# Kernel optimization log

Hardware: AMD Instinct MI355X
Metric: run time of the kernel (lower is better)

The kernel has to match this reference:

```python
import jax, jax.numpy as jnp
import numpy as np


def setup_inputs() -> dict:
    key = jax.random.key(0)
    ks = jax.random.split(key, 8)
    B, C, H, W = 4, 256, 56, 56
    Cq = C // 8
    s = 0.05  # small init scale for conv weights, like kaiming-ish for 1x1 convs
    return {
        "x": jax.random.normal(ks[0], (B, C, H, W), jnp.float32),
        "Wq": jax.random.normal(ks[1], (Cq, C), jnp.float32) * s,
        "bq": jax.random.normal(ks[2], (Cq,), jnp.float32) * s,
        "Wk": jax.random.normal(ks[3], (Cq, C), jnp.float32) * s,
        "bk": jax.random.normal(ks[4], (Cq,), jnp.float32) * s,
        "Wv": jax.random.normal(ks[5], (C, C), jnp.float32) * s,
        "bv": jax.random.normal(ks[6], (C,), jnp.float32) * s,
        "gamma": jax.random.normal(ks[7], (1,), jnp.float32),
    }


def reference(x, Wq, bq, Wk, bk, Wv, bv, gamma):
    B, C, H, W = x.shape
    N = H * W
    xf = x.reshape(B, C, N)  # flatten spatial

    # 1x1 convs == channel matmuls
    q = jnp.einsum('oc,bcn->bon', Wq, xf) + bq[None, :, None]   # [B,Cq,N]
    k = jnp.einsum('oc,bcn->bon', Wk, xf) + bk[None, :, None]   # [B,Cq,N]
    v = jnp.einsum('oc,bcn->bon', Wv, xf) + bv[None, :, None]   # [B,C,N]

    # lipschitz_norm from weights: u=||Q||_F, v=max row-norm of K^T, w=max row-norm of V^T
    u = jnp.linalg.norm(Wq)
    vn = jnp.max(jnp.linalg.norm(Wk.T, axis=1))
    wn = jnp.max(jnp.linalg.norm(Wv.T, axis=1))
    norm_value = jnp.maximum(u * vn, u * wn)  # maximum(u*v, v*u, u*w)

    # energy[b,i,j] = <q[:,i], k[:,j]>, scaled by custom Lipschitz norm
    energy = jnp.einsum('bci,bcj->bij', q, k) / norm_value      # [B,N,N]
    attention = jax.nn.softmax(energy, axis=-1)

    # out[b,c,i] = sum_j v[b,c,j] * attention[b,i,j]
    out = jnp.einsum('bcj,bij->bci', v, attention).reshape(B, C, H, W)

    # lipschitz_bound: exp(sqrt(3)) * sqrt(N/C) + 2*sqrt(6)
    bound = np.float32(np.exp(np.sqrt(3.0)) * np.sqrt(N / C) + 2.0 * np.sqrt(6.0))
    out = out / bound

    return gamma * out + x
```

## Files before the change

kernel.cpp:

```cpp
#include <hip/hip_runtime.h>

#define N_SP 3136
#define C_CH 256
#define CQ   32
#define NB   4
#define JT   64
#define NJT  49
#define QT   64
#define INV_BOUND 0.04051569f
#define LOG2E 1.44269504f

typedef __attribute__((ext_vector_type(8))) short bf16x8;
typedef __attribute__((ext_vector_type(4))) float f32x4;
typedef __attribute__((ext_vector_type(2))) long long l64x2;
typedef unsigned short u16;
typedef unsigned int   u32;
typedef unsigned char  u8;
typedef long long      l64;

#define MFMA16(a,b,c) __builtin_amdgcn_mfma_f32_16x16x32_bf16(a,b,c,0,0,0)
#define MFMA8(a,b,c)  __builtin_amdgcn_mfma_f32_16x16x32_bf8_fp8(a,b,c,0,0,0)

__device__ __forceinline__ u16 f2b(float f) {
    u32 u = __builtin_bit_cast(u32, f);
    u += 0x7fffu + ((u >> 16) & 1u);
    return (u16)(u >> 16);
}
__device__ __forceinline__ u8 f2fp8(float f) {
    return (u8)(__builtin_amdgcn_cvt_pk_fp8_f32(f, f, 0, false) & 0xff);
}
__device__ __forceinline__ void dma16(const void* g, void* l) {
    __builtin_amdgcn_global_load_lds((const __attribute__((address_space(1))) u32*)g,
                                     (__attribute__((address_space(3))) u32*)l, 16, 0, 0);
}

__global__ __launch_bounds__(256) void stage1_kernel(
    const float* __restrict__ x, const float* __restrict__ Wq,
    const float* __restrict__ Wk, const float* __restrict__ Wv,
    u8* __restrict__ xT, u8* __restrict__ Wqb, u8* __restrict__ Wkb,
    u8* __restrict__ Wvb, float* __restrict__ scale_out,
    float* __restrict__ kmax)
{
    __shared__ float smem[64 * 65];
    const int t = threadIdx.x;
    const int bid = blockIdx.x;

    if (bid < 784) {
        float (*tile)[65] = (float(*)[65])smem;
        const int xcd = bid & 7, slot = bid >> 3;
        const int b = xcd >> 1;
        const int i = slot * 2 + (xcd & 1);
        const int ct = i & 3, nt = i >> 2;
        const int c0 = ct * 64, n0 = nt * 64;
        const int cc = t >> 4, nn4 = (t & 15) * 4;
        #pragma unroll
        for (int k = 0; k < 4; ++k) {
            int cl = cc + k * 16;
            float4 v = *(const float4*)(x + (size_t)(b * C_CH + c0 + cl) * N_SP + n0 + nn4);
            tile[cl][nn4] = v.x; tile[cl][nn4 + 1] = v.y;
            tile[cl][nn4 + 2] = v.z; tile[cl][nn4 + 3] = v.w;
        }
        __syncthreads();
        const int c4 = (t & 15) * 4, nn = t >> 4;
        #pragma unroll
        for (int k = 0; k < 4; ++k) {
            int nl = nn + k * 16;
            ushort4 o;
            o.x = f2b(tile[c4 + 0][nl]); o.y = f2b(tile[c4 + 1][nl]);
            o.z = f2b(tile[c4 + 2][nl]); o.w = f2b(tile[c4 + 3][nl]);
            const int off = ((c0 + c4) * 2) ^ ((nl & 15) << 5);
            *(ushort4*)(xT + (size_t)(b * N_SP + n0 + nl) * 512 + off) = o;
        }
    } else if (bid < 864) {
        int idx = (bid - 784) * 256 + t;
        const float* src; u8* dst; int off;
        if (idx < 2048)      { src = Wq; dst = Wqb; off = idx; }
        else if (idx < 4096) { src = Wk; dst = Wkb; off = idx - 2048; }
        else                 { src = Wv; dst = Wvb; off = idx - 4096; }
        float4 v = *(const float4*)(src + off * 4);
        ushort4 o; o.x = f2b(v.x); o.y = f2b(v.y); o.z = f2b(v.z); o.w = f2b(v.w);
        const int row = off >> 6, inner = (off & 63) * 8;
        *(ushort4*)(dst + row * 512 + (inner ^ ((row & 15) << 5))) = o;
    } else {
        if (t < NB) kmax[t] = 0.f;
        float* red = smem;
        float u2 = 0.f;
        for (int i = t; i < CQ * C_CH; i += 256) { float w = Wq[i]; u2 += w * w; }
        red[t] = u2; __syncthreads();
        #pragma unroll
        for (int s = 128; s > 0; s >>= 1) { if (t < s) red[t] += red[t + s]; __syncthreads(); }
        float u2t = red[0]; __syncthreads();
        float vn2 = 0.f;
        for (int o = 0; o < CQ; ++o)   { float w = Wk[o * C_CH + t]; vn2 += w * w; }
        float wn2 = 0.f;
        for (int o = 0; o < C_CH; ++o) { float w = Wv[o * C_CH + t]; wn2 += w * w; }
        red[t] = fmaxf(vn2, wn2); __syncthreads();
        #pragma unroll
        for (int s = 128; s > 0; s >>= 1) { if (t < s) red[t] = fmaxf(red[t], red[t + s]); __syncthreads(); }
        if (t == 0) scale_out[0] = 1.0f / (sqrtf(u2t) * sqrtf(red[0]));
    }
}

__global__ __launch_bounds__(256) void qkv_mfma(
    const u8* __restrict__ xT, const u8* __restrict__ Wqb,
    const u8* __restrict__ Wkb, const u8* __restrict__ Wvb,
    const float* __restrict__ bq, const float* __restrict__ bk,
    const float* __restrict__ bv, const float* __restrict__ scale_p,
    u16* __restrict__ qT, u8* __restrict__ Kg, u8* __restrict__ Vg,
    float* __restrict__ qnorm, float* __restrict__ kmax)
{
    __shared__ __align__(16) u8 xTl[32768];
    __shared__ __align__(16) u8 Wl[32768];

    const int t = threadIdx.x;
    const int xcd = blockIdx.x & 7, slot = blockIdx.x >> 3;
    const int b = xcd >> 1;
    const int i = slot * 2 + (xcd & 1);
    if (i >= 245) return;
    const int split = i / 49, nt = i % 49;
    const int w = t >> 6, lane = t & 63, li = t & 15, g = (t >> 4) & 3;
    const int n = nt * 64 + w * 16 + li;
    const int r0 = (split - 1) * 64;
    const f32x4 zero = {0.f, 0.f, 0.f, 0.f};

    {
        const u8* xsrc = xT + (size_t)(b * N_SP + nt * 64) * 512;
        #pragma unroll
        for (int k = 0; k < 8; ++k)
            dma16(xsrc + w * 8192 + k * 1024 + lane * 16, xTl + w * 8192 + k * 1024);
        if (split == 0) {
            #pragma unroll
            for (int k = 0; k < 4; ++k)
                dma16(Wqb + w * 4096 + k * 1024 + lane * 16, Wl + w * 4096 + k * 1024);
            #pragma unroll
            for (int k = 0; k < 4; ++k)
                dma16(Wkb + w * 4096 + k * 1024 + lane * 16, Wl + 16384 + w * 4096 + k * 1024);
        } else {
            const u8* wsrc = Wvb + (size_t)r0 * 512;
            #pragma unroll
            for (int k = 0; k < 8; ++k)
                dma16(wsrc + w * 8192 + k * 1024 + lane * 16, Wl + w * 8192 + k * 1024);
        }
    }
    asm volatile("s_waitcnt vmcnt(0)" ::: "memory");
    __syncthreads();

    const int swz = li << 5;
    bf16x8 xf[8];
    #pragma unroll
    for (int ks = 0; ks < 8; ++ks)
        xf[ks] = *(const bf16x8*)(xTl + (w * 16 + li) * 512 + ((ks * 64 + 16 * g) ^ swz));

    if (split == 0) {
        f32x4 aq0 = zero, aq1 = zero, ak0 = zero, ak1 = zero;
        #pragma unroll
        for (int ks = 0; ks < 8; ++ks) {
            const int o = (ks * 64 + 16 * g) ^ swz;
            bf16x8 w0 = *(const bf16x8*)(Wl + li * 512 + o);
            bf16x8 w1 = *(const bf16x8*)(Wl + (16 + li) * 512 + o);
            bf16x8 w2 = *(const bf16x8*)(Wl + 16384 + li * 512 + o);
            bf16x8 w3 = *(const bf16x8*)(Wl + 16384 + (16 + li) * 512 + o);
            aq0 = MFMA16(w0, xf[ks], aq0);
            aq1 = MFMA16(w1, xf[ks], aq1);
            ak0 = MFMA16(w2, xf[ks], ak0);
            ak1 = MFMA16(w3, xf[ks], ak1);
        }
        const float scf = scale_p[0] * LOG2E;
        f32x4 bq0 = *(const f32x4*)(bq + 4 * g);
        f32x4 bq1 = *(const f32x4*)(bq + 16 + 4 * g);
        f32x4 bk0 = *(const f32x4*)(bk + 4 * g);
        f32x4 bk1 = *(const f32x4*)(bk + 16 + 4 * g);
        float qn2 = 0.f, kn2 = 0.f;
        ushort4 s0, s1;
        #pragma unroll
        for (int r = 0; r < 4; ++r) {
            float q0 = (aq0[r] + bq0[r]) * scf;
            float q1 = (aq1[r] + bq1[r]) * scf;
            qn2 += q0 * q0 + q1 * q1;
            ((u16*)&s0)[r] = f2b(q0); ((u16*)&s1)[r] = f2b(q1);
        }
        *(ushort4*)(qT + (size_t)(b * N_SP + n) * CQ + 4 * g)      = s0;
        *(ushort4*)(qT + (size_t)(b * N_SP + n) * CQ + 16 + 4 * g) = s1;
        #pragma unroll
        for (int r = 0; r < 4; ++r) {
            float k0 = ak0[r] + bk0[r];
            float k1 = ak1[r] + bk1[r];
            kn2 += k0 * k0 + k1 * k1;
            ((u16*)&s0)[r] = f2b(k0); ((u16*)&s1)[r] = f2b(k1);
        }
        u8* krow = Kg + ((size_t)b * N_SP + n) * 64;
        const int swn = ((n >> 1) & 3) << 4;
        *(ushort4*)(krow + ((8 * g) ^ swn))      = s0;
        *(ushort4*)(krow + ((32 + 8 * g) ^ swn)) = s1;

        qn2 += __shfl_xor(qn2, 16); qn2 += __shfl_xor(qn2, 32);
        kn2 += __shfl_xor(kn2, 16); kn2 += __shfl_xor(kn2, 32);
        if (g == 0) qnorm[b * N_SP + n] = sqrtf(qn2);
        float kn = sqrtf(kn2);
        #pragma unroll
        for (int d = 1; d < 16; d <<= 1) kn = fmaxf(kn, __shfl_xor(kn, d));
        if ((t & 63) == 0) atomicMax((int*)(kmax + b), __float_as_int(kn));
    } else {
        f32x4 a[4] = {zero, zero, zero, zero};
        #pragma unroll
        for (int ks = 0; ks < 8; ++ks) {
            const int o = (ks * 64 + 16 * g) ^ swz;
            #pragma unroll
            for (int fr = 0; fr < 4; ++fr) {
                bf16x8 wf = *(const bf16x8*)(Wl + (fr * 16 + li) * 512 + o);
                a[fr] = MFMA16(wf, xf[ks], a[fr]);
            }
        }
        const int jj = w * 16 + li;
        const int p = ((jj >> 5) & 1) * 8 + ((jj >> 3) & 3) * 16 + (jj & 7);
        u8* vtile = Vg + (size_t)(b * NJT + nt) * 16384;
        #pragma unroll
        for (int fr = 0; fr < 4; ++fr) {
            f32x4 bb = *(const f32x4*)(bv + r0 + fr * 16 + 4 * g);
            #pragma unroll
            for (int r = 0; r < 4; ++r) {
                const int c = r0 + fr * 16 + 4 * g + r;
                vtile[c * 64 + (p ^ (((c >> 1) & 3) << 4))] = f2fp8(a[fr][r] + bb[r]);
            }
        }
    }
}

__global__ __launch_bounds__(1024) void attn_mfma(
    const u16* __restrict__ qT, const u8* __restrict__ Kg,
    const u8* __restrict__ Vg, const float* __restrict__ x,
    const float* __restrict__ gamma_p, const float* __restrict__ qnorm,
    const float* __restrict__ kmax, float* __restrict__ out)
{
    __shared__ __align__(16) u8 smem[90112];
    u8* const Vl = smem;
    u8* const Kl = smem + 65536;
    u8* const Pl = smem + 81920;

    const int t = threadIdx.x;
    const int w = t >> 6, li = t & 15, g = (t >> 4) & 3;
    const int jh = w & 3, qh = w >> 2;
    const int swz = ((li >> 1) & 3) << 4;

    const int b  = blockIdx.x / NJT;
    const int qt = blockIdx.x % NJT;
    const int i0 = qt * QT;

    const u16* qTb = qT + (size_t)b * N_SP * CQ;
    const u8*  Kbb = Kg + (size_t)b * N_SP * 64;
    const u8*  Vbb = Vg + (size_t)b * NJT * 16384;
    const float kmb = kmax[b];
    const f32x4 zero = {0.f, 0.f, 0.f, 0.f};

    const bf16x8 qf = *(const bf16x8*)(qTb + (size_t)(i0 + qh * 16 + li) * CQ + 8 * g);
    const float  mr = qnorm[b * N_SP + i0 + qh * 16 + li] * kmb;

    f32x4 acc[4];
    #pragma unroll
    for (int qq = 0; qq < 4; ++qq) acc[qq] = zero;
    float ls = 0.f;

    #define ISSUE(jt_, s_) do {                                               \
        dma16(Vbb + (size_t)(jt_) * 16384 + t * 16,                           \
              Vl + (s_) * 16384 + w * 1024);                                  \
        if (t < 256)                                                          \
            dma16(Kbb + (size_t)(jt_) * 4096 + t * 16,                        \
                  Kl + (s_) * 4096 + w * 1024);                               \
    } while (0)

    #define SPHASE(it_) do {                                                  \
        const u8* Kc_ = Kl + ((it_) & 3) * 4096;                              \
        bf16x8 kf_ = *(const bf16x8*)(Kc_ + (jh * 16 + li) * 64 + ((16 * g) ^ swz)); \
        f32x4 s_ = MFMA16(kf_, qf, zero);                                     \
        float a0_ = exp2f(s_[0] - mr), a1_ = exp2f(s_[1] - mr);               \
        float a2_ = exp2f(s_[2] - mr), a3_ = exp2f(s_[3] - mr);               \
        ls += (a0_ + a1_) + (a2_ + a3_);                                      \
        int pk_ = __builtin_amdgcn_cvt_pk_bf8_f32(a0_, a1_, 0, false);        \
        pk_ = __builtin_amdgcn_cvt_pk_bf8_f32(a2_, a3_, pk_, true);           \
        *(u32*)(Pl + ((it_) & 1) * 4096 + (qh * 16 + li) * 64 + (p0 ^ swz)) = (u32)pk_; \
    } while (0)

    #define PVPHASE(it_) do {                                                 \
        const u8* Pp_ = Pl + ((it_) & 1) * 4096;                              \
        const u8* Vc_ = Vl + ((it_) & 3) * 16384;                             \
        __builtin_amdgcn_s_setprio(1);                                        \
        l64x2 pa0_ = *(const l64x2*)(Pp_ + (0 * 16 + li) * 64 + ((16 * g) ^ swz)); \
        l64x2 pa1_ = *(const l64x2*)(Pp_ + (1 * 16 + li) * 64 + ((16 * g) ^ swz)); \
        l64x2 pa2_ = *(const l64x2*)(Pp_ + (2 * 16 + li) * 64 + ((16 * g) ^ swz)); \
        l64x2 pa3_ = *(const l64x2*)(Pp_ + (3 * 16 + li) * 64 + ((16 * g) ^ swz)); \
        l64x2 v0_  = *(const l64x2*)(Vc_ + (w * 16 + li) * 64 + ((16 * g) ^ swz)); \
        acc[0] = MFMA8(pa0_[0], v0_[0], acc[0]);                              \
        acc[1] = MFMA8(pa1_[0], v0_[0], acc[1]);                              \
        acc[2] = MFMA8(pa2_[0], v0_[0], acc[2]);                              \
        acc[3] = MFMA8(pa3_[0], v0_[0], acc[3]);                              \
        acc[0] = MFMA8(pa0_[1], v0_[1], acc[0]);                              \
        acc[1] = MFMA8(pa1_[1], v0_[1], acc[1]);                              \
        acc[2] = MFMA8(pa2_[1], v0_[1], acc[2]);                              \
        acc[3] = MFMA8(pa3_[1], v0_[1], acc[3]);                              \
        __builtin_amdgcn_s_setprio(0);                                        \
    } while (0)

    ISSUE(0, 0);
    ISSUE(1, 1);

    const int p0 = ((jh >> 1) & 1) * 8 + ((jh * 2 + (g >> 1)) & 3) * 16 + 4 * (g & 1);

    if (w < 4) asm volatile("s_waitcnt vmcnt(2) lgkmcnt(0)" ::: "memory");
    else       asm volatile("s_waitcnt vmcnt(1) lgkmcnt(0)" ::: "memory");
    __builtin_amdgcn_s_barrier();
    asm volatile("" ::: "memory");
    ISSUE(2, 2);
    SPHASE(0);

    for (int it = 1; it < NJT; ++it) {
        if (w < 4) asm volatile("s_waitcnt vmcnt(2) lgkmcnt(0)" ::: "memory");
        else       asm volatile("s_waitcnt vmcnt(1) lgkmcnt(0)" ::: "memory");
        __builtin_amdgcn_s_barrier();
        asm volatile("" ::: "memory");
        {
            int jn = it + 2; if (jn > NJT - 1) jn = NJT - 1;
            ISSUE(jn, (it + 2) & 3);
        }
        PVPHASE(it - 1);
        SPHASE(it);
    }

    asm volatile("s_waitcnt lgkmcnt(0)" ::: "memory");
    __builtin_amdgcn_s_barrier();
    asm volatile("" ::: "memory");
    PVPHASE(NJT - 1);
    #undef ISSUE
    #undef SPHASE
    #undef PVPHASE

    ls += __shfl_xor(ls, 16); ls += __shfl_xor(ls, 32);
    __syncthreads();
    float* red       = (float*)Pl;
    float* red_final = (float*)(Pl + 1024);
    if ((t & 63) < 16) red[w * 16 + li] = ls;
    __syncthreads();
    if (t < 64) {
        const int qh2 = t >> 4, l2 = t & 15;
        float s = red[(qh2 * 4 + 0) * 16 + l2] + red[(qh2 * 4 + 1) * 16 + l2]
                + red[(qh2 * 4 + 2) * 16 + l2] + red[(qh2 * 4 + 3) * 16 + l2];
        red_final[t] = s;
    }
    __syncthreads();

    const float gsc = gamma_p[0] * INV_BOUND;
    const int c = w * 16 + li;
    #pragma unroll
    for (int qq = 0; qq < 4; ++qq) {
        f32x4 lsv = *(const f32x4*)(red_final + qq * 16 + 4 * g);
        f32x4 rinv;
        #pragma unroll
        for (int r = 0; r < 4; ++r) rinv[r] = gsc / lsv[r];
        const size_t base = ((size_t)b * C_CH + c) * N_SP + i0 + qq * 16 + 4 * g;
        float4 xv = *(const float4*)(x + base);
        float4 o;
        o.x = acc[qq][0] * rinv[0] + xv.x;
        o.y = acc[qq][1] * rinv[1] + xv.y;
        o.z = acc[qq][2] * rinv[2] + xv.z;
        o.w = acc[qq][3] * rinv[3] + xv.w;
        *(float4*)(out + base) = o;
    }
}

extern "C" void kernel_launch(void* const* d_in, const int* in_sizes, int n_in,
                              void* d_out, int out_size, void* d_ws, size_t ws_size,
                              hipStream_t stream)
{
    const float* x  = (const float*)d_in[0];
    const float* Wq = (const float*)d_in[1];
    const float* bq = (const float*)d_in[2];
    const float* Wk = (const float*)d_in[3];
    const float* bk = (const float*)d_in[4];
    const float* Wv = (const float*)d_in[5];
    const float* bv = (const float*)d_in[6];
    const float* gm = (const float*)d_in[7];
    float* out = (float*)d_out;
    float* ws  = (float*)d_ws;

    float* scale = ws;
    float* kmax  = ws + 4;
    float* qnorm = ws + 8;
    u8* Wqb = (u8*)(ws + 8 + NB * N_SP);
    u8* Wkb = Wqb + 32 * 512;
    u8* Wvb = Wkb + 32 * 512;
    u8* xT  = Wvb + 256 * 512;
    u16* qT = (u16*)(xT + (size_t)NB * N_SP * 512);
    u8* Kg  = (u8*)(qT + (size_t)NB * N_SP * CQ);
    u8* Vg  = Kg + (size_t)NB * N_SP * 64;

    stage1_kernel<<<865, 256, 0, stream>>>(x, Wq, Wk, Wv, xT, Wqb, Wkb, Wvb, scale, kmax);
    qkv_mfma<<<984, 256, 0, stream>>>(xT, Wqb, Wkb, Wvb, bq, bk, bv, scale, qT, Kg, Vg, qnorm, kmax);
    attn_mfma<<<196, 1024, 0, stream>>>(qT, Kg, Vg, x, gm, qnorm, kmax, out);
}
```

Measured before the change: 82.31 us.

## Fuse x transpose/bf16 conversion into QKV projection kernel, one block per tile

Result: no change. 81.32 us (-1.2%).

```diff
diff --git a/kernel.cpp b/kernel.cpp
--- a/kernel.cpp
+++ b/kernel.cpp
@@ -34,45 +34,18 @@
                                      (__attribute__((address_space(3))) u32*)l, 16, 0, 0);
 }
 
-__global__ __launch_bounds__(256) void stage1_kernel(
-    const float* __restrict__ x, const float* __restrict__ Wq,
-    const float* __restrict__ Wk, const float* __restrict__ Wv,
-    u8* __restrict__ xT, u8* __restrict__ Wqb, u8* __restrict__ Wkb,
-    u8* __restrict__ Wvb, float* __restrict__ scale_out,
-    float* __restrict__ kmax)
+__global__ __launch_bounds__(256) void stage0_kernel(
+    const float* __restrict__ Wq, const float* __restrict__ Wk,
+    const float* __restrict__ Wv, u8* __restrict__ Wqb,
+    u8* __restrict__ Wkb, u8* __restrict__ Wvb,
+    float* __restrict__ scale_out, float* __restrict__ kmax)
 {
-    __shared__ float smem[64 * 65];
+    __shared__ float red[256];
     const int t = threadIdx.x;
     const int bid = blockIdx.x;
 
-    if (bid < 784) {
-        float (*tile)[65] = (float(*)[65])smem;
-        const int xcd = bid & 7, slot = bid >> 3;
-        const int b = xcd >> 1;
-        const int i = slot * 2 + (xcd & 1);
-        const int ct = i & 3, nt = i >> 2;
-        const int c0 = ct * 64, n0 = nt * 64;
-        const int cc = t >> 4, nn4 = (t & 15) * 4;
-        #pragma unroll
-        for (int k = 0; k < 4; ++k) {
-            int cl = cc + k * 16;
-            float4 v = *(const float4*)(x + (size_t)(b * C_CH + c0 + cl) * N_SP + n0 + nn4);
-            tile[cl][nn4] = v.x; tile[cl][nn4 + 1] = v.y;
-            tile[cl][nn4 + 2] = v.z; tile[cl][nn4 + 3] = v.w;
-        }
-        __syncthreads();
-        const int c4 = (t & 15) * 4, nn = t >> 4;
-        #pragma unroll
-        for (int k = 0; k < 4; ++k) {
-            int nl = nn + k * 16;
-            ushort4 o;
-            o.x = f2b(tile[c4 + 0][nl]); o.y = f2b(tile[c4 + 1][nl]);
-            o.z = f2b(tile[c4 + 2][nl]); o.w = f2b(tile[c4 + 3][nl]);
-            const int off = ((c0 + c4) * 2) ^ ((nl & 15) << 5);
-            *(ushort4*)(xT + (size_t)(b * N_SP + n0 + nl) * 512 + off) = o;
-        }
-    } else if (bid < 864) {
-        int idx = (bid - 784) * 256 + t;
+    if (bid < 80) {
+        int idx = bid * 256 + t;
         const float* src; u8* dst; int off;
         if (idx < 2048)      { src = Wq; dst = Wqb; off = idx; }
         else if (idx < 4096) { src = Wk; dst = Wkb; off = idx - 2048; }
@@ -83,7 +56,6 @@
         *(ushort4*)(dst + row * 512 + (inner ^ ((row & 15) << 5))) = o;
     } else {
         if (t < NB) kmax[t] = 0.f;
-        float* red = smem;
         float u2 = 0.f;
         for (int i = t; i < CQ * C_CH; i += 256) { float w = Wq[i]; u2 += w * w; }
         red[t] = u2; __syncthreads();
@@ -101,76 +73,94 @@
     }
 }
 
-__global__ __launch_bounds__(256) void qkv_mfma(
-    const u8* __restrict__ xT, const u8* __restrict__ Wqb,
+__global__ __launch_bounds__(512) void qkv_fused(
+    const float* __restrict__ x, const u8* __restrict__ Wqb,
     const u8* __restrict__ Wkb, const u8* __restrict__ Wvb,
     const float* __restrict__ bq, const float* __restrict__ bk,
     const float* __restrict__ bv, const float* __restrict__ scale_p,
     u16* __restrict__ qT, u8* __restrict__ Kg, u8* __restrict__ Vg,
     float* __restrict__ qnorm, float* __restrict__ kmax)
 {
-    __shared__ __align__(16) u8 xTl[32768];
-    __shared__ __align__(16) u8 Wl[32768];
+    __shared__ __align__(16) u8 smem[147712];
+    u8* const xTl = smem;
+    float* const ftile = (float*)(smem + 32768);
+    u8* const W0 = smem + 49408;
+    u8* const W1 = smem + 82176;
 
     const int t = threadIdx.x;
-    const int xcd = blockIdx.x & 7, slot = blockIdx.x >> 3;
-    const int b = xcd >> 1;
-    const int i = slot * 2 + (xcd & 1);
-    if (i >= 245) return;
-    const int split = i / 49, nt = i % 49;
     const int w = t >> 6, lane = t & 63, li = t & 15, g = (t >> 4) & 3;
-    const int n = nt * 64 + w * 16 + li;
-    const int r0 = (split - 1) * 64;
+    const int wq = w & 3, wh = w >> 2;
+    const int b  = blockIdx.x / NJT;
+    const int nt = blockIdx.x % NJT;
+    const int n0 = nt * 64;
     const f32x4 zero = {0.f, 0.f, 0.f, 0.f};
 
-    {
-        const u8* xsrc = xT + (size_t)(b * N_SP + nt * 64) * 512;
-        #pragma unroll
-        for (int k = 0; k < 8; ++k)
-            dma16(xsrc + w * 8192 + k * 1024 + lane * 16, xTl + w * 8192 + k * 1024);
-        if (split == 0) {
-            #pragma unroll
-            for (int k = 0; k < 4; ++k)
-                dma16(Wqb + w * 4096 + k * 1024 + lane * 16, Wl + w * 4096 + k * 1024);
-            #pragma unroll
-            for (int k = 0; k < 4; ++k)
-                dma16(Wkb + w * 4096 + k * 1024 + lane * 16, Wl + 16384 + w * 4096 + k * 1024);
-        } else {
-            const u8* wsrc = Wvb + (size_t)r0 * 512;
-            #pragma unroll
-            for (int k = 0; k < 8; ++k)
-                dma16(wsrc + w * 8192 + k * 1024 + lane * 16, Wl + w * 8192 + k * 1024);
-        }
-    }
-    asm volatile("s_waitcnt vmcnt(0)" ::: "memory");
+    #pragma unroll
+    for (int k = 0; k < 2; ++k)
+        dma16(Wqb + k * 8192 + t * 16, W0 + k * 8192 + w * 1024);
+    #pragma unroll
+    for (int k = 0; k < 2; ++k)
+        dma16(Wkb + k * 8192 + t * 16, W0 + 16384 + k * 8192 + w * 1024);
+    #pragma unroll
+    for (int k = 0; k < 8; ++k)
+        dma16(Wvb + k * 8192 + t * 16, W1 + k * 8192 + w * 1024);
+
+    #pragma unroll 1
+    for (int sl = 0; sl < 4; ++sl) {
+        const int c0 = sl * 64;
+        if (t < 256) {
+            const int cc = t >> 4, nn4 = (t & 15) * 4;
+            #pragma unroll
+            for (int k = 0; k < 4; ++k) {
+                int cl = cc + k * 16;
+                float4 v = *(const float4*)(x + (size_t)(b * C_CH + c0 + cl) * N_SP + n0 + nn4);
+                ftile[cl * 65 + nn4]     = v.x;
+                ftile[cl * 65 + nn4 + 1] = v.y;
+                ftile[cl * 65 + nn4 + 2] = v.z;
+                ftile[cl * 65 + nn4 + 3] = v.w;
+            }
+        }
+        __syncthreads();
+        if (t < 256) {
+            const int c4 = (t & 15) * 4, nn = t >> 4;
+            #pragma unroll
+            for (int k = 0; k < 4; ++k) {
+                int nl = nn + k * 16;
+                ushort4 o;
+                o.x = f2b(ftile[(c4 + 0) * 65 + nl]);
+                o.y = f2b(ftile[(c4 + 1) * 65 + nl]);
+                o.z = f2b(ftile[(c4 + 2) * 65 + nl]);
+                o.w = f2b(ftile[(c4 + 3) * 65 + nl]);
+                *(ushort4*)(xTl + nl * 512 + (((c0 + c4) * 2) ^ ((nl & 15) << 5))) = o;
+            }
+        }
+        __syncthreads();
+    }
+
+    asm volatile("s_waitcnt vmcnt(0) lgkmcnt(0)" ::: "memory");
     __syncthreads();
 
     const int swz = li << 5;
+    const int n = n0 + wq * 16 + li;
     bf16x8 xf[8];
     #pragma unroll
     for (int ks = 0; ks < 8; ++ks)
-        xf[ks] = *(const bf16x8*)(xTl + (w * 16 + li) * 512 + ((ks * 64 + 16 * g) ^ swz));
-
-    if (split == 0) {
-        f32x4 aq0 = zero, aq1 = zero, ak0 = zero, ak1 = zero;
+        xf[ks] = *(const bf16x8*)(xTl + (wq * 16 + li) * 512 + ((ks * 64 + 16 * g) ^ swz));
+
+    if (wh == 0) {
+        f32x4 aq0 = zero, aq1 = zero;
         #pragma unroll
         for (int ks = 0; ks < 8; ++ks) {
             const int o = (ks * 64 + 16 * g) ^ swz;
-            bf16x8 w0 = *(const bf16x8*)(Wl + li * 512 + o);
-            bf16x8 w1 = *(const bf16x8*)(Wl + (16 + li) * 512 + o);
-            bf16x8 w2 = *(const bf16x8*)(Wl + 16384 + li * 512 + o);
-            bf16x8 w3 = *(const bf16x8*)(Wl + 16384 + (16 + li) * 512 + o);
+            bf16x8 w0 = *(const bf16x8*)(W0 + li * 512 + o);
+            bf16x8 w1 = *(const bf16x8*)(W0 + (16 + li) * 512 + o);
             aq0 = MFMA16(w0, xf[ks], aq0);
             aq1 = MFMA16(w1, xf[ks], aq1);
-            ak0 = MFMA16(w2, xf[ks], ak0);
-            ak1 = MFMA16(w3, xf[ks], ak1);
         }
         const float scf = scale_p[0] * LOG2E;
         f32x4 bq0 = *(const f32x4*)(bq + 4 * g);
         f32x4 bq1 = *(const f32x4*)(bq + 16 + 4 * g);
-        f32x4 bk0 = *(const f32x4*)(bk + 4 * g);
-        f32x4 bk1 = *(const f32x4*)(bk + 16 + 4 * g);
-        float qn2 = 0.f, kn2 = 0.f;
+        float qn2 = 0.f;
         ushort4 s0, s1;
         #pragma unroll
         for (int r = 0; r < 4; ++r) {
@@ -181,6 +171,22 @@
         }
         *(ushort4*)(qT + (size_t)(b * N_SP + n) * CQ + 4 * g)      = s0;
         *(ushort4*)(qT + (size_t)(b * N_SP + n) * CQ + 16 + 4 * g) = s1;
+        qn2 += __shfl_xor(qn2, 16); qn2 += __shfl_xor(qn2, 32);
+        if (g == 0) qnorm[b * N_SP + n] = sqrtf(qn2);
+    } else {
+        f32x4 ak0 = zero, ak1 = zero;
+        #pragma unroll
+        for (int ks = 0; ks < 8; ++ks) {
+            const int o = (ks * 64 + 16 * g) ^ swz;
+            bf16x8 w2 = *(const bf16x8*)(W0 + 16384 + li * 512 + o);
+            bf16x8 w3 = *(const bf16x8*)(W0 + 16384 + (16 + li) * 512 + o);
+            ak0 = MFMA16(w2, xf[ks], ak0);
+            ak1 = MFMA16(w3, xf[ks], ak1);
+        }
+        f32x4 bk0 = *(const f32x4*)(bk + 4 * g);
+        f32x4 bk1 = *(const f32x4*)(bk + 16 + 4 * g);
+        float kn2 = 0.f;
+        ushort4 s0, s1;
         #pragma unroll
         for (int r = 0; r < 4; ++r) {
             float k0 = ak0[r] + bk0[r];
@@ -192,34 +198,65 @@
         const int swn = ((n >> 1) & 3) << 4;
         *(ushort4*)(krow + ((8 * g) ^ swn))      = s0;
         *(ushort4*)(krow + ((32 + 8 * g) ^ swn)) = s1;
-
-        qn2 += __shfl_xor(qn2, 16); qn2 += __shfl_xor(qn2, 32);
         kn2 += __shfl_xor(kn2, 16); kn2 += __shfl_xor(kn2, 32);
-        if (g == 0) qnorm[b * N_SP + n] = sqrtf(qn2);
         float kn = sqrtf(kn2);
         #pragma unroll
         for (int d = 1; d < 16; d <<= 1) kn = fmaxf(kn, __shfl_xor(kn, d));
-        if ((t & 63) == 0) atomicMax((int*)(kmax + b), __float_as_int(kn));
-    } else {
+        if (lane == 0) atomicMax((int*)(kmax + b), __float_as_int(kn));
+    }
+
+    const int jj = wq * 16 + li;
+    const int p = ((jj >> 5) & 1) * 8 + ((jj >> 3) & 3) * 16 + (jj & 7);
+    u8* vtile = Vg + (size_t)(b * NJT + nt) * 16384;
+    {
+        const int r0 = wh * 64;
         f32x4 a[4] = {zero, zero, zero, zero};
         #pragma unroll
         for (int ks = 0; ks < 8; ++ks) {
             const int o = (ks * 64 + 16 * g) ^ swz;
             #pragma unroll
             for (int fr = 0; fr < 4; ++fr) {
-                bf16x8 wf = *(const bf16x8*)(Wl + (fr * 16 + li) * 512 + o);
+                bf16x8 wf = *(const bf16x8*)(W1 + (size_t)(r0 + fr * 16 + li) * 512 + o);
                 a[fr] = MFMA16(wf, xf[ks], a[fr]);
             }
         }
-        const int jj = w * 16 + li;
-        const int p = ((jj >> 5) & 1) * 8 + ((jj >> 3) & 3) * 16 + (jj & 7);
-        u8* vtile = Vg + (size_t)(b * NJT + nt) * 16384;
         #pragma unroll
         for (int fr = 0; fr < 4; ++fr) {
             f32x4 bb = *(const f32x4*)(bv + r0 + fr * 16 + 4 * g);
             #pragma unroll
             for (int r = 0; r < 4; ++r) {
                 const int c = r0 + fr * 16 + 4 * g + r;
+                vtile[c * 64 + (p ^ (((c >> 1) & 3) << 4))] = f2fp8(a[fr][r] + bb[r]);
+            }
+        }
+    }
+
+    __syncthreads();
+    #pragma unroll
+    for (int k = 0; k < 8; ++k)
+        dma16(Wvb + 65536 + k * 8192 + t * 16, W1 + k * 8192 + w * 1024);
+    asm volatile("s_waitcnt vmcnt(0)" ::: "memory");
+    __syncthreads();
+
+    {
+        const int r0v = 128 + wh * 64;
+        const int r0l = wh * 64;
+        f32x4 a[4] = {zero, zero, zero, zero};
+        #pragma unroll
+        for (int ks = 0; ks < 8; ++ks) {
+            const int o = (ks * 64 + 16 * g) ^ swz;
+            #pragma unroll
+            for (int fr = 0; fr < 4; ++fr) {
+                bf16x8 wf = *(const bf16x8*)(W1 + (size_t)(r0l + fr * 16 + li) * 512 + o);
+                a[fr] = MFMA16(wf, xf[ks], a[fr]);
+            }
+        }
+        #pragma unroll
+        for (int fr = 0; fr < 4; ++fr) {
+            f32x4 bb = *(const f32x4*)(bv + r0v + fr * 16 + 4 * g);
+            #pragma unroll
+            for (int r = 0; r < 4; ++r) {
+                const int c = r0v + fr * 16 + 4 * g + r;
                 vtile[c * 64 + (p ^ (((c >> 1) & 3) << 4))] = f2fp8(a[fr][r] + bb[r]);
             }
         }
@@ -387,12 +424,11 @@
     u8* Wqb = (u8*)(ws + 8 + NB * N_SP);
     u8* Wkb = Wqb + 32 * 512;
     u8* Wvb = Wkb + 32 * 512;
-    u8* xT  = Wvb + 256 * 512;
-    u16* qT = (u16*)(xT + (size_t)NB * N_SP * 512);
+    u16* qT = (u16*)(Wvb + 256 * 512);
     u8* Kg  = (u8*)(qT + (size_t)NB * N_SP * CQ);
     u8* Vg  = Kg + (size_t)NB * N_SP * 64;
 
-    stage1_kernel<<<865, 256, 0, stream>>>(x, Wq, Wk, Wv, xT, Wqb, Wkb, Wvb, scale, kmax);
-    qkv_mfma<<<984, 256, 0, stream>>>(xT, Wqb, Wkb, Wvb, bq, bk, bv, scale, qT, Kg, Vg, qnorm, kmax);
-    attn_mfma<<<196, 1024, 0, stream>>>(qT, Kg, Vg, x, gm, qnorm, kmax, out);
-}
+    stage0_kernel<<<81, 256, 0, stream>>>(Wq, Wk, Wv, Wqb, Wkb, Wvb, scale, kmax);
+    qkv_fused<<<NB * NJT, 512, 0, stream>>>(x, Wqb, Wkb, Wvb, bq, bk, bv, scale, qT, Kg, Vg, qnorm, kmax);
+    attn_mfma<<<NB * NJT, 1024, 0, stream>>>(qT, Kg, Vg, x, gm, qnorm, kmax, out);
+}
```
